# Kernel optimization log

Hardware: AMD Instinct MI355X
Metric: run time of the kernel (lower is better)

Reference implementation:

```python
import jax, jax.numpy as jnp
import numpy as np

B = 8192
I_SIZE = 1024
H_SIZE = 1024
C2 = 2.7183  # module's hard-coded e approximation

def setup_inputs() -> dict:
    key = jax.random.key(0)
    k0, k1, k2, k3, k4 = jax.random.split(key, 5)
    input_tensor = jax.random.uniform(k0, (B, I_SIZE + 1), dtype=jnp.float32)  # last col = dt >= 0
    h_cur = jax.random.normal(k1, (B, H_SIZE), dtype=jnp.float32)
    c_cur = jax.random.normal(k2, (B, H_SIZE), dtype=jnp.float32)
    W_layers = jax.random.normal(k3, (4 * H_SIZE, I_SIZE + H_SIZE), dtype=jnp.float32) * 0.02
    b_layers = jnp.zeros((4 * H_SIZE,), dtype=jnp.float32)
    W_desc = jax.random.normal(k4, (H_SIZE, H_SIZE), dtype=jnp.float32) * 0.02
    b_desc = jnp.zeros((H_SIZE,), dtype=jnp.float32)
    return {"input_tensor": input_tensor, "h_cur": h_cur, "c_cur": c_cur,
            "W_layers": W_layers, "b_layers": b_layers,
            "W_desc": W_desc, "b_desc": b_desc}

def reference(input_tensor, h_cur, c_cur, W_layers, b_layers, W_desc, b_desc):
    x = input_tensor[:, :-1]          # [B, I]
    dt = input_tensor[:, -1:]         # [B, 1]
    # map_elapse_time: T = 1/log(t + e), broadcast over h_size (matmul with ones == broadcast)
    T = 1.0 / jnp.log(dt + C2)        # [B, 1]
    C_ST = jnp.tanh(h_cur @ W_desc.T + b_desc)          # [B, H]
    h_adj = h_cur - C_ST + T * C_ST                     # decayed short-term memory
    combined = jnp.concatenate([x, h_adj], axis=1)      # [B, I+H]
    gates = combined @ W_layers.T + b_layers            # [B, 4H]
    cc_i, cc_f, cc_o, cc_g = jnp.split(gates, 4, axis=1)
    i = jax.nn.sigmoid(cc_i)
    f = jax.nn.sigmoid(cc_f)
    o = jax.nn.sigmoid(cc_o)
    g = jnp.tanh(cc_g)
    c_next = f * c_cur + i * g
    h_next = o * jnp.tanh(c_next)
    return (h_next, c_next)
```

## Files before the change

### kernel.cpp

```cpp
#include <hip/hip_runtime.h>
#include <hip/hip_bf16.h>
#include <math.h>

typedef __bf16 bf16x8 __attribute__((ext_vector_type(8)));
typedef float  f32x4  __attribute__((ext_vector_type(4)));

#define B_ROWS 8192
#define HSZ    1024

#define GLOAD16(gsrc, ldst)                                                          \
  __builtin_amdgcn_global_load_lds((const __attribute__((address_space(1))) void*)(gsrc), \
                                   (__attribute__((address_space(3))) void*)(ldst),  \
                                   16, 0, 0)

__device__ inline unsigned short f2bf(float f) {
  union { float f; unsigned u; } x; x.f = f;
  unsigned r = x.u + 0x7fffu + ((x.u >> 16) & 1u);
  return (unsigned short)(r >> 16);
}

__device__ inline void store4bf(unsigned short* p, float4 v) {
  ushort4 u;
  u.x = f2bf(v.x); u.y = f2bf(v.y); u.z = f2bf(v.z); u.w = f2bf(v.w);
  *(ushort4*)p = u;
}

__device__ inline float sigm(float x) { return 1.0f / (1.0f + __expf(-x)); }

__global__ void k_convert(const float* __restrict__ inp,
                          const float* __restrict__ h,
                          const float* __restrict__ Wl,
                          const float* __restrict__ Wd,
                          unsigned short* __restrict__ comb,
                          unsigned short* __restrict__ Wlb,
                          unsigned short* __restrict__ hb,
                          unsigned short* __restrict__ Wdb,
                          float* __restrict__ Tm1) {
  const long stride = (long)gridDim.x * blockDim.x;
  const long tid0 = (long)blockIdx.x * blockDim.x + threadIdx.x;

  for (long i = tid0; i < (long)B_ROWS * HSZ / 4; i += stride) {
    float4 v = ((const float4*)h)[i];
    store4bf(hb + i * 4, v);
  }
  for (long i = tid0; i < (long)B_ROWS * HSZ / 4; i += stride) {
    long e = i * 4; long b = e >> 10; long c = e & 1023;
    float4 v = *(const float4*)(inp + b * 1025 + c);
    store4bf(comb + b * 2048 + c, v);
  }
  for (long i = tid0; i < 4096L * 2048 / 4; i += stride) {
    float4 v = ((const float4*)Wl)[i];
    store4bf(Wlb + i * 4, v);
  }
  for (long i = tid0; i < 1024L * 1024 / 4; i += stride) {
    float4 v = ((const float4*)Wd)[i];
    store4bf(Wdb + i * 4, v);
  }
  for (long i = tid0; i < B_ROWS; i += stride) {
    float dt = inp[i * 1025 + 1024];
    Tm1[i] = 1.0f / logf(dt + 2.7183f) - 1.0f;
  }
}

__global__ void k_gemm1(const unsigned short* __restrict__ A,
                        const unsigned short* __restrict__ Bm,
                        const float* __restrict__ h,
                        const float* __restrict__ bd,
                        const float* __restrict__ Tm1,
                        unsigned short* __restrict__ comb) {
  const int K = 1024;
  __shared__ __align__(16) unsigned short As[128 * 32];
  __shared__ __align__(16) unsigned short Bs[128 * 32];
  const int tid = threadIdx.x;
  const int lane = tid & 63;
  const int wave = tid >> 6;
  const int wr = wave >> 1, wc = wave & 1;
  const int bRow = blockIdx.x;
  const int bCol = blockIdx.y;

  const int sRow = tid >> 2;
  const int sK = (tid & 3) * 8;
  const unsigned short* aSrc0 = A + (long)(bRow * 128 + sRow) * K + sK;
  const unsigned short* aSrc1 = A + (long)(bRow * 128 + 64 + sRow) * K + sK;
  const unsigned short* bSrc0 = Bm + (long)(bCol * 128 + sRow) * K + sK;
  const unsigned short* bSrc1 = Bm + (long)(bCol * 128 + 64 + sRow) * K + sK;
  unsigned short* aDst0 = As + tid * 8;
  unsigned short* aDst1 = As + 2048 + tid * 8;
  unsigned short* bDst0 = Bs + tid * 8;
  unsigned short* bDst1 = Bs + 2048 + tid * 8;

  f32x4 acc[4][4] = {};
  const int fr = lane & 15, fk = (lane >> 4) * 8;

  for (int k0 = 0; k0 < K; k0 += 32) {
    GLOAD16(aSrc0 + k0, aDst0);
    GLOAD16(aSrc1 + k0, aDst1);
    GLOAD16(bSrc0 + k0, bDst0);
    GLOAD16(bSrc1 + k0, bDst1);
    __syncthreads();
    bf16x8 a[4], b[4];
#pragma unroll
    for (int m = 0; m < 4; m++) a[m] = *(const bf16x8*)(As + (wr * 64 + m * 16 + fr) * 32 + fk);
#pragma unroll
    for (int n = 0; n < 4; n++) b[n] = *(const bf16x8*)(Bs + (wc * 64 + n * 16 + fr) * 32 + fk);
#pragma unroll
    for (int m = 0; m < 4; m++)
#pragma unroll
      for (int n = 0; n < 4; n++)
        acc[m][n] = __builtin_amdgcn_mfma_f32_16x16x32_bf16(a[m], b[n], acc[m][n], 0, 0, 0);
    __syncthreads();
  }

  const int cr = (lane >> 4) * 4;
  const int cc = lane & 15;
#pragma unroll
  for (int m = 0; m < 4; m++)
#pragma unroll
    for (int n = 0; n < 4; n++) {
      const int col = bCol * 128 + wc * 64 + n * 16 + cc;
#pragma unroll
      for (int r = 0; r < 4; r++) {
        const int row = bRow * 128 + wr * 64 + m * 16 + cr + r;
        float v = acc[m][n][r] + bd[col];
        float cst = tanhf(v);
        float hadj = h[(long)row * HSZ + col] + Tm1[row] * cst;
        comb[(long)row * 2048 + 1024 + col] = f2bf(hadj);
      }
    }
}

#define NT2 64
__global__ __launch_bounds__(512, 2)
void k_gemm2_8ph(const unsigned short* __restrict__ A,
                 const unsigned short* __restrict__ Bm,
                 const float* __restrict__ bl,
                 const float* __restrict__ c_cur,
                 float* __restrict__ out) {
  __shared__ __align__(16) unsigned short lds[4][16384];

  const int tid = threadIdx.x;
  const int lane = tid & 63;
  const int wid = tid >> 6;
  const int wr = wid >> 2;
  const int wc = wid & 3;

  const int bid = blockIdx.x;
  const int swz = (bid & 7) * 64 + (bid >> 3);
  const int bRow = swz & 31;
  const int bCol = swz >> 5;

  const int sr = tid >> 2;
  const int swsel = (sr >> 1) & 3;
  const int gk = ((tid & 3) ^ swsel) << 3;
  const unsigned short* aBase = A + (long)(bRow * 256 + sr) * 2048 + gk;
  const int rl0 = sr, rl1 = 128 + sr;
  const int grow0 = ((rl0 >> 4) & 3) * 1024 + bCol * 64 + (rl0 >> 6) * 16 + (rl0 & 15);
  const int grow1 = ((rl1 >> 4) & 3) * 1024 + bCol * 64 + (rl1 >> 6) * 16 + (rl1 & 15);
  const unsigned short* bBase0 = Bm + (long)grow0 * 2048 + gk;
  const unsigned short* bBase1 = Bm + (long)grow1 * 2048 + gk;

#define STAGE_A2(tt) { unsigned short* d_ = &lds[(tt) & 3][0] + tid * 8;          \
    GLOAD16(aBase + (long)(tt) * 32, d_);                                          \
    GLOAD16(aBase + 128L * 2048 + (long)(tt) * 32, d_ + 512 * 8); }
#define STAGE_B2(tt) { unsigned short* d_ = &lds[(tt) & 3][8192] + tid * 8;       \
    GLOAD16(bBase0 + (long)(tt) * 32, d_);                                         \
    GLOAD16(bBase1 + (long)(tt) * 32, d_ + 512 * 8); }

  const int fr = lane & 15, q = lane >> 4;
  int offA[8], offB[4];
#pragma unroll
  for (int m = 0; m < 8; m++) {
    const int row = wr * 128 + m * 16 + fr;
    offA[m] = row * 32 + ((q ^ ((row >> 1) & 3)) << 3);
  }
#pragma unroll
  for (int n = 0; n < 4; n++) {
    const int row = wc * 64 + n * 16 + fr;
    offB[n] = 8192 + row * 32 + ((q ^ ((row >> 1) & 3)) << 3);
  }

  f32x4 acc[8][4] = {};

  STAGE_A2(0); STAGE_B2(0);
  STAGE_A2(1); STAGE_B2(1);
  STAGE_A2(2); STAGE_B2(2);
  asm volatile("s_waitcnt vmcnt(8)" ::: "memory");
  __builtin_amdgcn_sched_barrier(0);
  __builtin_amdgcn_s_barrier();

  for (int t = 0; t < NT2; ++t) {
    const unsigned short* buf = lds[t & 3];
    bf16x8 a[4], b[4];
#pragma unroll
    for (int m = 0; m < 4; m++) a[m] = *(const bf16x8*)(buf + offA[m]);
#pragma unroll
    for (int n = 0; n < 4; n++) b[n] = *(const bf16x8*)(buf + offB[n]);
    if (t < NT2 - 3) STAGE_A2(t + 3);
    __builtin_amdgcn_s_barrier();
    asm volatile("s_waitcnt lgkmcnt(0)" ::: "memory");
    __builtin_amdgcn_sched_barrier(0);
    __builtin_amdgcn_s_setprio(1);
#pragma unroll
    for (int m = 0; m < 4; m++)
#pragma unroll
      for (int n = 0; n < 4; n++)
        acc[m][n] = __builtin_amdgcn_mfma_f32_16x16x32_bf16(a[m], b[n], acc[m][n], 0, 0, 0);
    __builtin_amdgcn_s_setprio(0);
    __builtin_amdgcn_s_barrier();
#pragma unroll
    for (int m = 0; m < 4; m++) a[m] = *(const bf16x8*)(buf + offA[m + 4]);
    if (t < NT2 - 3) STAGE_B2(t + 3);
    __builtin_amdgcn_s_barrier();
    asm volatile("s_waitcnt lgkmcnt(0)" ::: "memory");
    __builtin_amdgcn_sched_barrier(0);
    __builtin_amdgcn_s_setprio(1);
#pragma unroll
    for (int m = 0; m < 4; m++)
#pragma unroll
      for (int n = 0; n < 4; n++)
        acc[m + 4][n] = __builtin_amdgcn_mfma_f32_16x16x32_bf16(a[m], b[n], acc[m + 4][n], 0, 0, 0);
    __builtin_amdgcn_s_setprio(0);
    if (t < NT2 - 3)       { asm volatile("s_waitcnt vmcnt(8)" ::: "memory"); }
    else if (t == NT2 - 3) { asm volatile("s_waitcnt vmcnt(4)" ::: "memory"); }
    else if (t == NT2 - 2) { asm volatile("s_waitcnt vmcnt(0)" ::: "memory"); }
    __builtin_amdgcn_sched_barrier(0);
    __builtin_amdgcn_s_barrier();
  }

  const int cr = (lane >> 4) * 4;
  const int cc = lane & 15;
  const int j = bCol * 64 + wc * 16 + cc;
#pragma unroll
  for (int m = 0; m < 8; m++) {
#pragma unroll
    for (int r = 0; r < 4; r++) {
      const int row = bRow * 256 + wr * 128 + m * 16 + cr + r;
      float iv = sigm(acc[m][0][r] + bl[j]);
      float fv = sigm(acc[m][1][r] + bl[1024 + j]);
      float ov = sigm(acc[m][2][r] + bl[2048 + j]);
      float gv = tanhf(acc[m][3][r] + bl[3072 + j]);
      float cn = fv * c_cur[(long)row * HSZ + j] + iv * gv;
      float hn = ov * tanhf(cn);
      out[(long)row * HSZ + j] = hn;
      out[(long)B_ROWS * HSZ + (long)row * HSZ + j] = cn;
    }
  }
}

extern "C" void kernel_launch(void* const* d_in, const int* in_sizes, int n_in,
                              void* d_out, int out_size, void* d_ws, size_t ws_size,
                              hipStream_t stream) {
  const float* inp = (const float*)d_in[0];
  const float* h   = (const float*)d_in[1];
  const float* c   = (const float*)d_in[2];
  const float* Wl  = (const float*)d_in[3];
  const float* bl  = (const float*)d_in[4];
  const float* Wd  = (const float*)d_in[5];
  const float* bd  = (const float*)d_in[6];

  char* ws = (char*)d_ws;
  unsigned short* comb = (unsigned short*)(ws);
  unsigned short* Wlb  = (unsigned short*)(ws + 33554432);
  unsigned short* hb   = (unsigned short*)(ws + 50331648);
  unsigned short* Wdb  = (unsigned short*)(ws + 67108864);
  float*          Tm1  = (float*)(ws + 69206016);
  float*          out  = (float*)d_out;

  hipLaunchKernelGGL(k_convert, dim3(2048), dim3(256), 0, stream,
                     inp, h, Wl, Wd, comb, Wlb, hb, Wdb, Tm1);
  hipLaunchKernelGGL(k_gemm1, dim3(64, 8), dim3(256), 0, stream,
                     hb, Wdb, h, bd, Tm1, comb);
  hipLaunchKernelGGL(k_gemm2_8ph, dim3(512), dim3(512), 0, stream,
                     comb, Wlb, bl, c, out);
}
```

Before: 243.0 us.

## Software-pipeline LDS fragment loads across K tiles in the gate GEMM

Result: faster. 234.4 us (-3.5%).

```diff
diff --git a/kernel.cpp b/kernel.cpp
--- a/kernel.cpp
+++ b/kernel.cpp
@@ -131,11 +131,11 @@
 
 #define NT2 64
 __global__ __launch_bounds__(512, 2)
-void k_gemm2_8ph(const unsigned short* __restrict__ A,
-                 const unsigned short* __restrict__ Bm,
-                 const float* __restrict__ bl,
-                 const float* __restrict__ c_cur,
-                 float* __restrict__ out) {
+void k_gemm2_pipe(const unsigned short* __restrict__ A,
+                  const unsigned short* __restrict__ Bm,
+                  const float* __restrict__ bl,
+                  const float* __restrict__ c_cur,
+                  float* __restrict__ out) {
   __shared__ __align__(16) unsigned short lds[4][16384];
 
   const int tid = threadIdx.x;
@@ -180,6 +180,7 @@
   }
 
   f32x4 acc[8][4] = {};
+  bf16x8 aL0[4], aL1[4], b0[4], b1[4], aH[4];
 
   STAGE_A2(0); STAGE_B2(0);
   STAGE_A2(1); STAGE_B2(1);
@@ -187,45 +188,56 @@
   asm volatile("s_waitcnt vmcnt(8)" ::: "memory");
   __builtin_amdgcn_sched_barrier(0);
   __builtin_amdgcn_s_barrier();
-
-  for (int t = 0; t < NT2; ++t) {
-    const unsigned short* buf = lds[t & 3];
-    bf16x8 a[4], b[4];
-#pragma unroll
-    for (int m = 0; m < 4; m++) a[m] = *(const bf16x8*)(buf + offA[m]);
-#pragma unroll
-    for (int n = 0; n < 4; n++) b[n] = *(const bf16x8*)(buf + offB[n]);
-    if (t < NT2 - 3) STAGE_A2(t + 3);
-    __builtin_amdgcn_s_barrier();
-    asm volatile("s_waitcnt lgkmcnt(0)" ::: "memory");
-    __builtin_amdgcn_sched_barrier(0);
-    __builtin_amdgcn_s_setprio(1);
-#pragma unroll
-    for (int m = 0; m < 4; m++)
-#pragma unroll
-      for (int n = 0; n < 4; n++)
-        acc[m][n] = __builtin_amdgcn_mfma_f32_16x16x32_bf16(a[m], b[n], acc[m][n], 0, 0, 0);
-    __builtin_amdgcn_s_setprio(0);
-    __builtin_amdgcn_s_barrier();
-#pragma unroll
-    for (int m = 0; m < 4; m++) a[m] = *(const bf16x8*)(buf + offA[m + 4]);
-    if (t < NT2 - 3) STAGE_B2(t + 3);
-    __builtin_amdgcn_s_barrier();
-    asm volatile("s_waitcnt lgkmcnt(0)" ::: "memory");
-    __builtin_amdgcn_sched_barrier(0);
-    __builtin_amdgcn_s_setprio(1);
-#pragma unroll
-    for (int m = 0; m < 4; m++)
-#pragma unroll
-      for (int n = 0; n < 4; n++)
-        acc[m + 4][n] = __builtin_amdgcn_mfma_f32_16x16x32_bf16(a[m], b[n], acc[m + 4][n], 0, 0, 0);
-    __builtin_amdgcn_s_setprio(0);
-    if (t < NT2 - 3)       { asm volatile("s_waitcnt vmcnt(8)" ::: "memory"); }
-    else if (t == NT2 - 3) { asm volatile("s_waitcnt vmcnt(4)" ::: "memory"); }
-    else if (t == NT2 - 2) { asm volatile("s_waitcnt vmcnt(0)" ::: "memory"); }
-    __builtin_amdgcn_sched_barrier(0);
-    __builtin_amdgcn_s_barrier();
-  }
+  __builtin_amdgcn_sched_barrier(0);
+#pragma unroll
+  for (int m = 0; m < 4; m++) aL0[m] = *(const bf16x8*)(&lds[0][0] + offA[m]);
+#pragma unroll
+  for (int n = 0; n < 4; n++) b0[n] = *(const bf16x8*)(&lds[0][0] + offB[n]);
+
+#define TILE_BODY(t, aC, bC, aN, bN)                                                 \
+  {                                                                                  \
+    const unsigned short* buf = lds[(t) & 3];                                        \
+    _Pragma("unroll")                                                                \
+    for (int m = 0; m < 4; m++) aH[m] = *(const bf16x8*)(buf + offA[m + 4]);         \
+    if ((t) < NT2 - 3) STAGE_A2((t) + 3);                                            \
+    __builtin_amdgcn_sched_barrier(0);                                               \
+    __builtin_amdgcn_s_setprio(1);                                                   \
+    _Pragma("unroll")                                                                \
+    for (int m = 0; m < 4; m++)                                                      \
+      _Pragma("unroll")                                                              \
+      for (int n = 0; n < 4; n++)                                                    \
+        acc[m][n] = __builtin_amdgcn_mfma_f32_16x16x32_bf16(aC[m], bC[n], acc[m][n], 0, 0, 0); \
+    __builtin_amdgcn_s_setprio(0);                                                   \
+    asm volatile("s_waitcnt lgkmcnt(0)" ::: "memory");                               \
+    if ((t) < NT2 - 3)        { asm volatile("s_waitcnt vmcnt(6)" ::: "memory"); }   \
+    else if ((t) == NT2 - 3)  { asm volatile("s_waitcnt vmcnt(4)" ::: "memory"); }   \
+    else                      { asm volatile("s_waitcnt vmcnt(0)" ::: "memory"); }   \
+    __builtin_amdgcn_sched_barrier(0);                                               \
+    __builtin_amdgcn_s_barrier();                                                    \
+    __builtin_amdgcn_sched_barrier(0);                                               \
+    if ((t) < NT2 - 1) {                                                             \
+      const unsigned short* bufN = lds[((t) + 1) & 3];                               \
+      _Pragma("unroll")                                                              \
+      for (int m = 0; m < 4; m++) aN[m] = *(const bf16x8*)(bufN + offA[m]);          \
+      _Pragma("unroll")                                                              \
+      for (int n = 0; n < 4; n++) bN[n] = *(const bf16x8*)(bufN + offB[n]);          \
+      if ((t) < NT2 - 3) STAGE_B2((t) + 3);                                          \
+    }                                                                                \
+    __builtin_amdgcn_sched_barrier(0);                                               \
+    __builtin_amdgcn_s_setprio(1);                                                   \
+    _Pragma("unroll")                                                                \
+    for (int m = 0; m < 4; m++)                                                      \
+      _Pragma("unroll")                                                              \
+      for (int n = 0; n < 4; n++)                                                    \
+        acc[m + 4][n] = __builtin_amdgcn_mfma_f32_16x16x32_bf16(aH[m], bC[n], acc[m + 4][n], 0, 0, 0); \
+    __builtin_amdgcn_s_setprio(0);                                                   \
+  }
+
+  for (int t = 0; t < NT2; t += 2) {
+    TILE_BODY(t,     aL0, b0, aL1, b1);
+    TILE_BODY(t + 1, aL1, b1, aL0, b0);
+  }
+#undef TILE_BODY
 
   const int cr = (lane >> 4) * 4;
   const int cc = lane & 15;
@@ -270,6 +282,6 @@
                      inp, h, Wl, Wd, comb, Wlb, hb, Wdb, Tm1);
   hipLaunchKernelGGL(k_gemm1, dim3(64, 8), dim3(256), 0, stream,
                      hb, Wdb, h, bd, Tm1, comb);
-  hipLaunchKernelGGL(k_gemm2_8ph, dim3(512), dim3(512), 0, stream,
+  hipLaunchKernelGGL(k_gemm2_pipe, dim3(512), dim3(512), 0, stream,
                      comb, Wlb, bl, c, out);
 }
```
